# Optimization experiments

Hardware: AMD Instinct MI355X
Metric: run time of the kernel (lower is better)

## Reference

```python
import jax, jax.numpy as jnp
import numpy as np

B, S, D, H = 4, 2048, 1024, 16
DK = D // H  # 64

def setup_inputs() -> dict:
    key = jax.random.key(0)
    kq, kk, kv = jax.random.split(key, 3)
    q = jax.random.normal(kq, (B, S, D), dtype=jnp.float32)
    k = jax.random.normal(kk, (B, S, D), dtype=jnp.float32)
    v = jax.random.normal(kv, (B, S, D), dtype=jnp.float32)
    return {"q": q, "k": k, "v": v}

def reference(q, k, v):
    # [B,S,D] -> [B,H,S,DK]
    qh = q.reshape(B, S, H, DK).transpose(0, 2, 1, 3)
    kh = k.reshape(B, S, H, DK).transpose(0, 2, 1, 3)
    vh = v.reshape(B, S, H, DK).transpose(0, 2, 1, 3)
    scale = 1.0 / np.sqrt(DK).astype(np.float32)
    scores = jnp.einsum('bhqd,bhkd->bhqk', qh, kh) * scale  # [B,H,S,S]
    probs = jax.nn.softmax(scores, axis=-1)
    out = jnp.einsum('bhqk,bhkd->bhqd', probs, vh)  # [B,H,S,DK]
    # concat heads: [B,S,D]
    return out.transpose(0, 2, 1, 3).reshape(B, S, D)
```

## Files before the change

### kernel.cpp

```cpp
#include <hip/hip_runtime.h>

#define B_   4
#define S_   2048
#define D_   1024
#define H_   16
#define DKV  64
#define BM   128
#define BN   64
#define PITCH 72

typedef float f32x4 __attribute__((ext_vector_type(4)));
typedef short bf16x8 __attribute__((ext_vector_type(8)));
typedef unsigned short ushort8_t __attribute__((ext_vector_type(8)));

__device__ __forceinline__ unsigned short f2b(float f) {
  union { float f; unsigned int u; } x; x.f = f;
  unsigned int u = x.u;
  unsigned int r = u + 0x7FFFu + ((u >> 16) & 1u);
  return (unsigned short)(r >> 16);
}

__global__ __launch_bounds__(256)
void prep_kv_kernel(const float* __restrict__ k, const float* __restrict__ v,
                    unsigned short* __restrict__ kb, unsigned short* __restrict__ vt) {
  __shared__ unsigned int sT[64 * 33];
  const int tid = threadIdx.x;
  const int s0  = blockIdx.x * 64;
  const int bh  = blockIdx.y;
  const int b   = bh >> 4;
  const int h   = bh & 15;

  for (int it = 0; it < 4; ++it) {
    int id  = tid + it * 256;
    int r   = id >> 4;
    int c4  = (id & 15) << 2;
    const size_t goff = ((size_t)(b * S_ + s0 + r)) * D_ + h * DKV + c4;
    const float4 fk = *reinterpret_cast<const float4*>(k + goff);
    unsigned k01, k23;
    asm("v_cvt_pk_bf16_f32 %0, %1, %2" : "=v"(k01) : "v"(fk.x), "v"(fk.y));
    asm("v_cvt_pk_bf16_f32 %0, %1, %2" : "=v"(k23) : "v"(fk.z), "v"(fk.w));
    uint2 uk; uk.x = k01; uk.y = k23;
    *reinterpret_cast<uint2*>(kb + goff) = uk;

    const float4 fv = *reinterpret_cast<const float4*>(v + goff);
    unsigned v01, v23;
    asm("v_cvt_pk_bf16_f32 %0, %1, %2" : "=v"(v01) : "v"(fv.x), "v"(fv.y));
    asm("v_cvt_pk_bf16_f32 %0, %1, %2" : "=v"(v23) : "v"(fv.z), "v"(fv.w));
    sT[r * 33 + (c4 >> 1)]     = v01;
    sT[r * 33 + (c4 >> 1) + 1] = v23;
  }
  __syncthreads();
  const unsigned short* sTs = reinterpret_cast<const unsigned short*>(sT);
  for (int it = 0; it < 2; ++it) {
    int id = tid + it * 256;
    int d  = id >> 3;
    int s8 = (id & 7) << 3;
    ushort8_t u;
    for (int t = 0; t < 8; ++t) u[t] = sTs[(s8 + t) * 66 + d];
    *reinterpret_cast<ushort8_t*>(vt + ((size_t)(bh * DKV + d)) * S_ + s0 + s8) = u;
  }
}

__global__ __launch_bounds__(256, 4)
void mha_fast_kernel(const float* __restrict__ q,
                     const unsigned short* __restrict__ kb,
                     const unsigned short* __restrict__ vt,
                     float* __restrict__ out) {
  __shared__ __align__(16) unsigned short sK [BN  * PITCH];
  __shared__ __align__(16) unsigned short sVt[DKV * PITCH];

  const int tid  = threadIdx.x;
  const int wave = tid >> 6;
  const int lane = tid & 63;
  const int ln   = lane & 15;
  const int quad = lane >> 4;

  const int bh = blockIdx.x;
  const int b  = bh >> 4;
  const int h  = bh & 15;
  const int q0 = blockIdx.y * BM;

  const float* qg = q + (size_t)b * S_ * D_ + h * DKV;
  const unsigned short* kbase = kb + (size_t)b * S_ * D_ + h * DKV;
  const unsigned short* vbase = vt + (size_t)bh * DKV * S_;
  float* og = out + (size_t)b * S_ * D_ + h * DKV;

  const float qs = 0.125f * 1.44269504088896340736f;

  bf16x8 qf[2][2];
  for (int mt = 0; mt < 2; ++mt)
    for (int ks = 0; ks < 2; ++ks) {
      const float* base = qg + (size_t)(q0 + wave * 32 + mt * 16 + ln) * D_
                             + ks * 32 + quad * 8;
      const float4 f0 = *reinterpret_cast<const float4*>(base);
      const float4 f1 = *reinterpret_cast<const float4*>(base + 4);
      bf16x8 a;
      a[0] = (short)f2b(f0.x * qs); a[1] = (short)f2b(f0.y * qs);
      a[2] = (short)f2b(f0.z * qs); a[3] = (short)f2b(f0.w * qs);
      a[4] = (short)f2b(f1.x * qs); a[5] = (short)f2b(f1.y * qs);
      a[6] = (short)f2b(f1.z * qs); a[7] = (short)f2b(f1.w * qs);
      qf[mt][ks] = a;
    }

  float l_part[2] = {0.f, 0.f};
  f32x4 o[2][4];
  for (int mt = 0; mt < 2; ++mt)
    for (int dt = 0; dt < 4; ++dt) o[mt][dt] = (f32x4){0.f, 0.f, 0.f, 0.f};

  int n_[2], c8_[2];
  for (int it = 0; it < 2; ++it) {
    int id = tid + it * 256;
    n_[it]  = id >> 3;
    c8_[it] = (id & 7) << 3;
  }

  ushort8_t pk[2], pv[2];
  for (int it = 0; it < 2; ++it) {
    pk[it] = *reinterpret_cast<const ushort8_t*>(kbase + (size_t)n_[it] * D_ + c8_[it]);
    pv[it] = *reinterpret_cast<const ushort8_t*>(vbase + (size_t)n_[it] * S_ + c8_[it]);
  }

  for (int n0 = 0; n0 < S_; n0 += BN) {
    __syncthreads();

    for (int it = 0; it < 2; ++it) {
      *reinterpret_cast<ushort8_t*>(&sK [n_[it] * PITCH + c8_[it]]) = pk[it];
      *reinterpret_cast<ushort8_t*>(&sVt[n_[it] * PITCH + c8_[it]]) = pv[it];
    }
    __syncthreads();

    if (n0 + BN < S_) {
      for (int it = 0; it < 2; ++it) {
        pk[it] = *reinterpret_cast<const ushort8_t*>(
            kbase + (size_t)(n0 + BN + n_[it]) * D_ + c8_[it]);
        pv[it] = *reinterpret_cast<const ushort8_t*>(
            vbase + (size_t)n_[it] * S_ + (n0 + BN) + c8_[it]);
      }
    }

    bf16x8 pA[2][2];
    for (int g = 0; g < 2; ++g) {
      unsigned lo[2][2], hi[2][2];
      for (int t = 0; t < 2; ++t) {
        const int nt = g * 2 + t;
        bf16x8 kf0 = *reinterpret_cast<const bf16x8*>(&sK[(nt * 16 + ln) * PITCH + quad * 8]);
        bf16x8 kf1 = *reinterpret_cast<const bf16x8*>(&sK[(nt * 16 + ln) * PITCH + 32 + quad * 8]);
        for (int mt = 0; mt < 2; ++mt) {
          f32x4 acc = (f32x4){0.f, 0.f, 0.f, 0.f};
          acc = __builtin_amdgcn_mfma_f32_16x16x32_bf16(kf0, qf[mt][0], acc, 0, 0, 0);
          acc = __builtin_amdgcn_mfma_f32_16x16x32_bf16(kf1, qf[mt][1], acc, 0, 0, 0);
          float p0 = __builtin_amdgcn_exp2f(acc[0]);
          float p1 = __builtin_amdgcn_exp2f(acc[1]);
          float p2 = __builtin_amdgcn_exp2f(acc[2]);
          float p3 = __builtin_amdgcn_exp2f(acc[3]);
          l_part[mt] += (p0 + p1) + (p2 + p3);
          unsigned plo, phi;
          asm("v_cvt_pk_bf16_f32 %0, %1, %2" : "=v"(plo) : "v"(p0), "v"(p1));
          asm("v_cvt_pk_bf16_f32 %0, %1, %2" : "=v"(phi) : "v"(p2), "v"(p3));
          lo[mt][t] = plo; hi[mt][t] = phi;
        }
      }
      for (int mt = 0; mt < 2; ++mt) {
        unsigned x = lo[mt][0], y = lo[mt][1];
        asm("v_permlane32_swap_b32 %0, %1" : "+v"(x), "+v"(y));
        asm("v_permlane16_swap_b32 %0, %1" : "+v"(x), "+v"(y));
        unsigned u = hi[mt][0], w = hi[mt][1];
        asm("v_permlane32_swap_b32 %0, %1" : "+v"(u), "+v"(w));
        asm("v_permlane16_swap_b32 %0, %1" : "+v"(u), "+v"(w));
        union { unsigned u32[4]; bf16x8 v8; } pw;
        pw.u32[0] = x; pw.u32[1] = u; pw.u32[2] = y; pw.u32[3] = w;
        pA[mt][g] = pw.v8;
      }
    }

    for (int g = 0; g < 2; ++g) {
      for (int dt = 0; dt < 4; ++dt) {
        bf16x8 vf = *reinterpret_cast<const bf16x8*>(
            &sVt[(dt * 16 + ln) * PITCH + g * 32 + quad * 8]);
        for (int mt = 0; mt < 2; ++mt)
          o[mt][dt] = __builtin_amdgcn_mfma_f32_16x16x32_bf16(pA[mt][g], vf, o[mt][dt], 0, 0, 0);
      }
    }
  }

  for (int mt = 0; mt < 2; ++mt) {
    float l = l_part[mt];
    l += __shfl_xor(l, 16, 64);
    l += __shfl_xor(l, 32, 64);
    const float linv = 1.f / l;
    float invr[4];
    for (int r = 0; r < 4; ++r)
      invr[r] = __shfl(linv, quad * 4 + r, 64);
    float* orow = og + (size_t)(q0 + wave * 32 + mt * 16 + quad * 4) * D_;
    for (int r = 0; r < 4; ++r)
      for (int dt = 0; dt < 4; ++dt)
        orow[(size_t)r * D_ + dt * 16 + ln] = o[mt][dt][r] * invr[r];
  }
}

extern "C" void kernel_launch(void* const* d_in, const int* in_sizes, int n_in,
                              void* d_out, int out_size, void* d_ws, size_t ws_size,
                              hipStream_t stream) {
  const float* q = (const float*)d_in[0];
  const float* k = (const float*)d_in[1];
  const float* v = (const float*)d_in[2];
  float* out = (float*)d_out;

  unsigned short* kb = (unsigned short*)d_ws;
  unsigned short* vt = kb + (size_t)B_ * S_ * D_;

  prep_kv_kernel<<<dim3(S_ / 64, B_ * H_), dim3(256), 0, stream>>>(k, v, kb, vt);
  mha_fast_kernel<<<dim3(B_ * H_, S_ / BM), dim3(256), 0, stream>>>(q, kb, vt, out);
}
```

Baseline: 203.3 us.

## Load V fragments directly from global memory instead of staging through LDS

Drops the shared-memory buffer for transposed V. Each wave now reads its V MFMA fragments straight from global memory (L2) inside each 32-key group, and the P·V MFMAs are fused into that group loop. This removes the LDS stores and loads for V and halves the LDS footprint, which may raise occupancy. In exchange, all four waves redundantly fetch the same V data from global memory, and the load latency now sits inside the loop without explicit prefetch.

```diff
diff --git a/kernel.cpp b/kernel.cpp
--- a/kernel.cpp
+++ b/kernel.cpp
@@ -66,8 +66,7 @@
                      const unsigned short* __restrict__ kb,
                      const unsigned short* __restrict__ vt,
                      float* __restrict__ out) {
-  __shared__ __align__(16) unsigned short sK [BN  * PITCH];
-  __shared__ __align__(16) unsigned short sVt[DKV * PITCH];
+  __shared__ __align__(16) unsigned short sK[BN * PITCH];
 
   const int tid  = threadIdx.x;
   const int wave = tid >> 6;
@@ -114,32 +113,29 @@
     c8_[it] = (id & 7) << 3;
   }
 
-  ushort8_t pk[2], pv[2];
-  for (int it = 0; it < 2; ++it) {
+  ushort8_t pk[2];
+  for (int it = 0; it < 2; ++it)
     pk[it] = *reinterpret_cast<const ushort8_t*>(kbase + (size_t)n_[it] * D_ + c8_[it]);
-    pv[it] = *reinterpret_cast<const ushort8_t*>(vbase + (size_t)n_[it] * S_ + c8_[it]);
-  }
 
   for (int n0 = 0; n0 < S_; n0 += BN) {
     __syncthreads();
 
-    for (int it = 0; it < 2; ++it) {
-      *reinterpret_cast<ushort8_t*>(&sK [n_[it] * PITCH + c8_[it]]) = pk[it];
-      *reinterpret_cast<ushort8_t*>(&sVt[n_[it] * PITCH + c8_[it]]) = pv[it];
-    }
+    for (int it = 0; it < 2; ++it)
+      *reinterpret_cast<ushort8_t*>(&sK[n_[it] * PITCH + c8_[it]]) = pk[it];
     __syncthreads();
 
     if (n0 + BN < S_) {
-      for (int it = 0; it < 2; ++it) {
+      for (int it = 0; it < 2; ++it)
         pk[it] = *reinterpret_cast<const ushort8_t*>(
             kbase + (size_t)(n0 + BN + n_[it]) * D_ + c8_[it]);
-        pv[it] = *reinterpret_cast<const ushort8_t*>(
-            vbase + (size_t)n_[it] * S_ + (n0 + BN) + c8_[it]);
-      }
     }
 
-    bf16x8 pA[2][2];
     for (int g = 0; g < 2; ++g) {
+      bf16x8 vf[4];
+      for (int dt = 0; dt < 4; ++dt)
+        vf[dt] = *reinterpret_cast<const bf16x8*>(
+            vbase + (size_t)(dt * 16 + ln) * S_ + n0 + g * 32 + quad * 8);
+
       unsigned lo[2][2], hi[2][2];
       for (int t = 0; t < 2; ++t) {
         const int nt = g * 2 + t;
@@ -160,6 +156,8 @@
           lo[mt][t] = plo; hi[mt][t] = phi;
         }
       }
+
+      bf16x8 pA[2];
       for (int mt = 0; mt < 2; ++mt) {
         unsigned x = lo[mt][0], y = lo[mt][1];
         asm("v_permlane32_swap_b32 %0, %1" : "+v"(x), "+v"(y));
@@ -169,17 +167,12 @@
         asm("v_permlane16_swap_b32 %0, %1" : "+v"(u), "+v"(w));
         union { unsigned u32[4]; bf16x8 v8; } pw;
         pw.u32[0] = x; pw.u32[1] = u; pw.u32[2] = y; pw.u32[3] = w;
-        pA[mt][g] = pw.v8;
+        pA[mt] = pw.v8;
       }
-    }
-
-    for (int g = 0; g < 2; ++g) {
-      for (int dt = 0; dt < 4; ++dt) {
-        bf16x8 vf = *reinterpret_cast<const bf16x8*>(
-            &sVt[(dt * 16 + ln) * PITCH + g * 32 + quad * 8]);
+
+      for (int dt = 0; dt < 4; ++dt)
         for (int mt = 0; mt < 2; ++mt)
-          o[mt][dt] = __builtin_amdgcn_mfma_f32_16x16x32_bf16(pA[mt][g], vf, o[mt][dt], 0, 0, 0);
-      }
+          o[mt][dt] = __builtin_amdgcn_mfma_f32_16x16x32_bf16(pA[mt], vf[dt], o[mt][dt], 0, 0, 0);
     }
   }
 
```

New measurement: 257.2 us. +26.5%, slower.
